# Kernel optimization log

Measured on AMD Instinct MI355X. Metric: run time of the kernel, lower is better.

Reference implementation:

```python
import jax, jax.numpy as jnp
import numpy as np
from jax import lax

EPS = 1e-6

def setup_inputs() -> dict:
    key = jax.random.key(0)
    B, C, K, T = 32, 1, 128, 8000
    x = jax.random.uniform(key, (B, C, K, T), dtype=jnp.float32)
    # parameters exactly as in PCENLayer.__init__ (log of init values)
    log_s = jnp.full((1, 1, K), np.log(0.025), dtype=jnp.float32)
    log_alpha = jnp.full((1, 1, K, 1), np.log(0.8), dtype=jnp.float32)
    log_delta = jnp.full((1, 1, K, 1), np.log(10.0), dtype=jnp.float32)
    log_r = jnp.full((1, 1, K, 1), np.log(0.25), dtype=jnp.float32)
    return {"x": x, "log_s": log_s, "log_alpha": log_alpha,
            "log_delta": log_delta, "log_r": log_r}

def reference(x, log_s, log_alpha, log_delta, log_r):
    # x: [B, C, K, T]
    s = jax.nn.sigmoid(log_s)            # (1, 1, K) smoother coefficient
    init = x[..., 0]                     # init smoother from first frame

    def step(prev, xt):
        f = (1.0 - s) * prev + s * xt
        return f, f

    xs = jnp.moveaxis(x[..., 1:], -1, 0)             # (T-1, B, C, K)
    _, fs = lax.scan(step, init, xs)                 # (T-1, B, C, K)
    filtered = jnp.concatenate([init[None], fs], 0)  # (T, B, C, K)
    filtered = jnp.moveaxis(filtered, 0, -1)         # (B, C, K, T)

    alpha = jnp.exp(log_alpha)           # (1, 1, K, 1)
    delta = jnp.exp(log_delta)
    r = jnp.exp(log_r)
    return (x / (EPS + filtered) ** alpha + delta) ** r - delta ** r
```

## Files before the change

kernel.cpp:

```cpp
#include <hip/hip_runtime.h>
#include <math.h>


constexpr int   T_LEN = 8000;
constexpr int   CHUNK = 32;
constexpr int   NTH   = 256;
constexpr int   KDIM  = 128;
constexpr float EPS_F = 1e-6f;

__global__ __launch_bounds__(NTH) void pcen_kernel(
    const float* __restrict__ x,
    const float* __restrict__ log_s,
    const float* __restrict__ log_alpha,
    const float* __restrict__ log_delta,
    const float* __restrict__ log_r,
    float* __restrict__ out)
{
    const int seq  = blockIdx.x;
    const int k    = seq % KDIM;
    const int tid  = threadIdx.x;
    const int lane = tid & 63;
    const int wave = tid >> 6;

    const float s       = 1.0f / (1.0f + expf(-log_s[k]));
    const float a       = 1.0f - s;
    const float alpha   = expf(log_alpha[k]);
    const float delta   = expf(log_delta[k]);
    const float r       = expf(log_r[k]);
    const float delta_r = powf(delta, r);

    const float* xp = x   + (size_t)seq * T_LEN + tid * CHUNK;
    float*       op = out + (size_t)seq * T_LEN + tid * CHUNK;
    const bool active = (tid * CHUNK) < T_LEN;

    float xv[CHUNK];
    if (active) {
        #pragma unroll
        for (int j = 0; j < CHUNK / 4; ++j) {
            float4 v = ((const float4*)xp)[j];
            xv[4*j+0] = v.x; xv[4*j+1] = v.y; xv[4*j+2] = v.z; xv[4*j+3] = v.w;
        }
    }

    float A = 1.0f, B = 0.0f;
    if (active) {
        float f;
        if (tid == 0) {
            f = xv[0];
            #pragma unroll
            for (int j = 1; j < CHUNK; ++j) f = fmaf(a, f, s * xv[j]);
            A = 0.0f;
        } else {
            f = 0.0f;
            #pragma unroll
            for (int j = 0; j < CHUNK; ++j) f = fmaf(a, f, s * xv[j]);
            const float a2 = a * a, a4 = a2 * a2, a8 = a4 * a4, a16 = a8 * a8;
            A = a16 * a16;
        }
        B = f;
    }

    #pragma unroll
    for (int off = 1; off < 64; off <<= 1) {
        const float pA = __shfl_up(A, off, 64);
        const float pB = __shfl_up(B, off, 64);
        if (lane >= off) {
            B = fmaf(A, pB, B);
            A = A * pA;
        }
    }

    __shared__ float wAs[NTH / 64], wBs[NTH / 64];
    if (lane == 63) { wAs[wave] = A; wBs[wave] = B; }
    __syncthreads();

    float pA = 1.0f, pB = 0.0f;
    for (int w = 0; w < wave; ++w) {
        pB = fmaf(wAs[w], pB, wBs[w]);
        pA = wAs[w] * pA;
    }

    float eA = __shfl_up(A, 1, 64);
    float eB = __shfl_up(B, 1, 64);
    if (lane == 0) { eA = 1.0f; eB = 0.0f; }
    const float fin = fmaf(eA, pB, eB);

    if (active) {
        float f = fin;
        #pragma unroll
        for (int j = 0; j < CHUNK; ++j) {
            if (tid == 0 && j == 0) f = xv[0];
            else                    f = fmaf(a, f, s * xv[j]);
            const float lg  = __log2f(EPS_F + f);
            const float inv = exp2f(-alpha * lg);
            const float u   = fmaf(xv[j], inv, delta);
            xv[j] = exp2f(r * __log2f(u)) - delta_r;
        }
        #pragma unroll
        for (int j = 0; j < CHUNK / 4; ++j) {
            ((float4*)op)[j] = make_float4(xv[4*j+0], xv[4*j+1], xv[4*j+2], xv[4*j+3]);
        }
    }
}

extern "C" void kernel_launch(void* const* d_in, const int* in_sizes, int n_in,
                              void* d_out, int out_size, void* d_ws, size_t ws_size,
                              hipStream_t stream) {
    const float* x         = (const float*)d_in[0];
    const float* log_s     = (const float*)d_in[1];
    const float* log_alpha = (const float*)d_in[2];
    const float* log_delta = (const float*)d_in[3];
    const float* log_r     = (const float*)d_in[4];
    float* out = (float*)d_out;

    const int nseq = in_sizes[0] / T_LEN;
    pcen_kernel<<<nseq, NTH, 0, stream>>>(x, log_s, log_alpha, log_delta, log_r, out);
}
```

Baseline: 249.4 us.

## Stage sequence through padded LDS for coalesced loads and smaller per-thread chunks

Loads each 8000-sample sequence into shared memory with coalesced float4 accesses, padded with a stride of 17 to avoid bank conflicts, then runs the chunked scan from LDS. It halves the chunk to 16 and doubles the block to 512 threads, and writes results back through LDS with coalesced stores. The aim is to replace strided per-thread 128-byte global accesses with coalesced ones and to raise parallelism. In exchange it adds about 32KB of LDS per block, which limits occupancy, plus an extra barrier and LDS traffic.

Result: faster. 242.6 us (-2.7%).

```diff
diff --git a/kernel.cpp b/kernel.cpp
--- a/kernel.cpp
+++ b/kernel.cpp
@@ -2,11 +2,15 @@
 #include <math.h>
 
 
-constexpr int   T_LEN = 8000;
-constexpr int   CHUNK = 32;
-constexpr int   NTH   = 256;
-constexpr int   KDIM  = 128;
-constexpr float EPS_F = 1e-6f;
+constexpr int   T_LEN  = 8000;
+constexpr int   CHUNK  = 16;
+constexpr int   NTH    = 512;
+constexpr int   NWAVE  = NTH / 64;
+constexpr int   KDIM   = 128;
+constexpr int   NVEC4  = T_LEN / 4;
+constexpr int   PSTRIDE = CHUNK + 1;
+constexpr int   LDS_FLOATS = (T_LEN / CHUNK) * PSTRIDE;
+constexpr float EPS_F  = 1e-6f;
 
 __global__ __launch_bounds__(NTH) void pcen_kernel(
     const float* __restrict__ x,
@@ -16,6 +20,9 @@
     const float* __restrict__ log_r,
     float* __restrict__ out)
 {
+    __shared__ float lds[LDS_FLOATS];
+    __shared__ float wAs[NWAVE], wBs[NWAVE];
+
     const int seq  = blockIdx.x;
     const int k    = seq % KDIM;
     const int tid  = threadIdx.x;
@@ -29,33 +36,38 @@
     const float r       = expf(log_r[k]);
     const float delta_r = powf(delta, r);
 
-    const float* xp = x   + (size_t)seq * T_LEN + tid * CHUNK;
-    float*       op = out + (size_t)seq * T_LEN + tid * CHUNK;
-    const bool active = (tid * CHUNK) < T_LEN;
+    const float* xseq = x   + (size_t)seq * T_LEN;
+    float*       oseq = out + (size_t)seq * T_LEN;
 
-    float xv[CHUNK];
-    if (active) {
-        #pragma unroll
-        for (int j = 0; j < CHUNK / 4; ++j) {
-            float4 v = ((const float4*)xp)[j];
-            xv[4*j+0] = v.x; xv[4*j+1] = v.y; xv[4*j+2] = v.z; xv[4*j+3] = v.w;
-        }
+    #pragma unroll
+    for (int i = tid; i < NVEC4; i += NTH) {
+        float4 v = ((const float4*)xseq)[i];
+        const int e    = 4 * i;
+        const int slot = (e >> 4) * PSTRIDE + (e & 15);
+        lds[slot + 0] = v.x;
+        lds[slot + 1] = v.y;
+        lds[slot + 2] = v.z;
+        lds[slot + 3] = v.w;
     }
+    __syncthreads();
+
+    const bool active = tid < (T_LEN / CHUNK);
+    const int  base   = tid * PSTRIDE;
 
     float A = 1.0f, B = 0.0f;
     if (active) {
         float f;
         if (tid == 0) {
-            f = xv[0];
+            f = lds[base];
             #pragma unroll
-            for (int j = 1; j < CHUNK; ++j) f = fmaf(a, f, s * xv[j]);
+            for (int j = 1; j < CHUNK; ++j) f = fmaf(a, f, s * lds[base + j]);
             A = 0.0f;
         } else {
             f = 0.0f;
             #pragma unroll
-            for (int j = 0; j < CHUNK; ++j) f = fmaf(a, f, s * xv[j]);
-            const float a2 = a * a, a4 = a2 * a2, a8 = a4 * a4, a16 = a8 * a8;
-            A = a16 * a16;
+            for (int j = 0; j < CHUNK; ++j) f = fmaf(a, f, s * lds[base + j]);
+            const float a2 = a * a, a4 = a2 * a2, a8 = a4 * a4;
+            A = a8 * a8;
         }
         B = f;
     }
@@ -70,14 +82,12 @@
         }
     }
 
-    __shared__ float wAs[NTH / 64], wBs[NTH / 64];
     if (lane == 63) { wAs[wave] = A; wBs[wave] = B; }
     __syncthreads();
 
-    float pA = 1.0f, pB = 0.0f;
+    float pB = 0.0f;
     for (int w = 0; w < wave; ++w) {
         pB = fmaf(wAs[w], pB, wBs[w]);
-        pA = wAs[w] * pA;
     }
 
     float eA = __shfl_up(A, 1, 64);
@@ -89,17 +99,24 @@
         float f = fin;
         #pragma unroll
         for (int j = 0; j < CHUNK; ++j) {
-            if (tid == 0 && j == 0) f = xv[0];
-            else                    f = fmaf(a, f, s * xv[j]);
+            const float xj = lds[base + j];
+            if (tid == 0 && j == 0) f = xj;
+            else                    f = fmaf(a, f, s * xj);
             const float lg  = __log2f(EPS_F + f);
             const float inv = exp2f(-alpha * lg);
-            const float u   = fmaf(xv[j], inv, delta);
-            xv[j] = exp2f(r * __log2f(u)) - delta_r;
+            const float u   = fmaf(xj, inv, delta);
+            lds[base + j] = exp2f(r * __log2f(u)) - delta_r;
         }
-        #pragma unroll
-        for (int j = 0; j < CHUNK / 4; ++j) {
-            ((float4*)op)[j] = make_float4(xv[4*j+0], xv[4*j+1], xv[4*j+2], xv[4*j+3]);
-        }
+    }
+    __syncthreads();
+
+    #pragma unroll
+    for (int i = tid; i < NVEC4; i += NTH) {
+        const int e    = 4 * i;
+        const int slot = (e >> 4) * PSTRIDE + (e & 15);
+        float4 v = make_float4(lds[slot + 0], lds[slot + 1],
+                               lds[slot + 2], lds[slot + 3]);
+        ((float4*)oseq)[i] = v;
     }
 }
 
```

## Shrink per-thread chunk, use 1024-thread blocks with shuffle-based cross-wave scan

Applied to the files above, without the earlier changes.

Each thread now handles 8 timesteps instead of 32, and each block uses 1024 threads. The cross-wave carry combine becomes a parallel shuffle scan in wave 0 instead of a serial loop in every wave. Local partial filter values are kept in registers so the second pass needs one fma per element rather than re-running the recurrence. The aim is to cut per-thread serial work and register use and raise parallelism per sequence, at the cost of an extra block barrier and more scan levels.

Measured after the change: 237.3 us. 1.05x faster.

```diff
diff --git a/kernel.cpp b/kernel.cpp
--- a/kernel.cpp
+++ b/kernel.cpp
@@ -3,12 +3,14 @@
 
 
 constexpr int   T_LEN = 8000;
-constexpr int   CHUNK = 32;
-constexpr int   NTH   = 256;
+constexpr int   CHUNK = 8;
+constexpr int   NTH   = 1024;
+constexpr int   NWAVE = NTH / 64;
+constexpr int   NACT  = T_LEN / CHUNK;
 constexpr int   KDIM  = 128;
 constexpr float EPS_F = 1e-6f;
 
-__global__ __launch_bounds__(NTH) void pcen_kernel(
+__global__ __launch_bounds__(NTH, 8) void pcen_kernel(
     const float* __restrict__ x,
     const float* __restrict__ log_s,
     const float* __restrict__ log_alpha,
@@ -16,6 +18,8 @@
     const float* __restrict__ log_r,
     float* __restrict__ out)
 {
+    __shared__ float wAs[NWAVE], wBs[NWAVE];
+
     const int seq  = blockIdx.x;
     const int k    = seq % KDIM;
     const int tid  = threadIdx.x;
@@ -27,35 +31,35 @@
     const float alpha   = expf(log_alpha[k]);
     const float delta   = expf(log_delta[k]);
     const float r       = expf(log_r[k]);
-    const float delta_r = powf(delta, r);
+    const float delta_r = exp2f(r * __log2f(delta));
 
     const float* xp = x   + (size_t)seq * T_LEN + tid * CHUNK;
     float*       op = out + (size_t)seq * T_LEN + tid * CHUNK;
-    const bool active = (tid * CHUNK) < T_LEN;
+    const bool active = tid < NACT;
 
     float xv[CHUNK];
     if (active) {
-        #pragma unroll
-        for (int j = 0; j < CHUNK / 4; ++j) {
-            float4 v = ((const float4*)xp)[j];
-            xv[4*j+0] = v.x; xv[4*j+1] = v.y; xv[4*j+2] = v.z; xv[4*j+3] = v.w;
-        }
+        float4 v0 = ((const float4*)xp)[0];
+        float4 v1 = ((const float4*)xp)[1];
+        xv[0] = v0.x; xv[1] = v0.y; xv[2] = v0.z; xv[3] = v0.w;
+        xv[4] = v1.x; xv[5] = v1.y; xv[6] = v1.z; xv[7] = v1.w;
     }
 
+    float q[CHUNK];
     float A = 1.0f, B = 0.0f;
     if (active) {
         float f;
         if (tid == 0) {
-            f = xv[0];
+            f = xv[0]; q[0] = f;
             #pragma unroll
-            for (int j = 1; j < CHUNK; ++j) f = fmaf(a, f, s * xv[j]);
+            for (int j = 1; j < CHUNK; ++j) { f = fmaf(a, f, s * xv[j]); q[j] = f; }
             A = 0.0f;
         } else {
             f = 0.0f;
             #pragma unroll
-            for (int j = 0; j < CHUNK; ++j) f = fmaf(a, f, s * xv[j]);
-            const float a2 = a * a, a4 = a2 * a2, a8 = a4 * a4, a16 = a8 * a8;
-            A = a16 * a16;
+            for (int j = 0; j < CHUNK; ++j) { f = fmaf(a, f, s * xv[j]); q[j] = f; }
+            const float a2 = a * a, a4 = a2 * a2;
+            A = a4 * a4;
         }
         B = f;
     }
@@ -70,36 +74,44 @@
         }
     }
 
-    __shared__ float wAs[NTH / 64], wBs[NTH / 64];
     if (lane == 63) { wAs[wave] = A; wBs[wave] = B; }
     __syncthreads();
-
-    float pA = 1.0f, pB = 0.0f;
-    for (int w = 0; w < wave; ++w) {
-        pB = fmaf(wAs[w], pB, wBs[w]);
-        pA = wAs[w] * pA;
+    if (wave == 0) {
+        float cA = (lane < NWAVE) ? wAs[lane] : 1.0f;
+        float cB = (lane < NWAVE) ? wBs[lane] : 0.0f;
+        #pragma unroll
+        for (int off = 1; off < NWAVE; off <<= 1) {
+            const float pA = __shfl_up(cA, off, 64);
+            const float pB = __shfl_up(cB, off, 64);
+            if (lane >= off) {
+                cB = fmaf(cA, pB, cB);
+                cA = cA * pA;
+            }
+        }
+        if (lane < NWAVE - 1) { wAs[lane + 1] = cA; wBs[lane + 1] = cB; }
+        if (lane == 0)        { wAs[0] = 1.0f;      wBs[0] = 0.0f;      }
     }
+    __syncthreads();
 
     float eA = __shfl_up(A, 1, 64);
     float eB = __shfl_up(B, 1, 64);
     if (lane == 0) { eA = 1.0f; eB = 0.0f; }
-    const float fin = fmaf(eA, pB, eB);
+    float fin = fmaf(eA, wBs[wave], eB);
+    if (tid == 0) fin = 0.0f;
 
     if (active) {
-        float f = fin;
+        float pw = a;
         #pragma unroll
         for (int j = 0; j < CHUNK; ++j) {
-            if (tid == 0 && j == 0) f = xv[0];
-            else                    f = fmaf(a, f, s * xv[j]);
+            const float f   = fmaf(pw, fin, q[j]);
+            pw *= a;
             const float lg  = __log2f(EPS_F + f);
             const float inv = exp2f(-alpha * lg);
             const float u   = fmaf(xv[j], inv, delta);
             xv[j] = exp2f(r * __log2f(u)) - delta_r;
         }
-        #pragma unroll
-        for (int j = 0; j < CHUNK / 4; ++j) {
-            ((float4*)op)[j] = make_float4(xv[4*j+0], xv[4*j+1], xv[4*j+2], xv[4*j+3]);
-        }
+        ((float4*)op)[0] = make_float4(xv[0], xv[1], xv[2], xv[3]);
+        ((float4*)op)[1] = make_float4(xv[4], xv[5], xv[6], xv[7]);
     }
 }
 
```
